# Optimization experiments

Hardware: AMD Instinct MI355X
Metric: run time of the kernel (lower is better)

## Reference

```python
import jax, jax.numpy as jnp
import numpy as np

BN_EPS = 1e-3  # keras BatchNormalization default epsilon

@jax.custom_vjp
def ste_sign(x):
    # larq ste_sign: sign(x) with sign(0) -> +1
    return jnp.where(x >= 0, 1.0, -1.0).astype(x.dtype)

def _ste_fwd(x):
    return ste_sign(x), x

def _ste_bwd(x, g):
    # straight-through estimator, gradient clipped to |x| <= 1
    return (g * (jnp.abs(x) <= 1).astype(g.dtype),)

ste_sign.defvjp(_ste_fwd, _ste_bwd)

def setup_inputs() -> dict:
    key = jax.random.key(0)
    k1, k2, k3, k4, k5, k6 = jax.random.split(key, 6)
    B, D_IN, D_H = 32768, 2048, 512
    return {
        "input_tensor": jax.random.normal(k1, (B, D_IN), dtype=jnp.float32),
        "W": jax.random.normal(k2, (D_IN, D_H), dtype=jnp.float32) * 0.05,
        "b": jax.random.normal(k3, (D_H,), dtype=jnp.float32) * 0.01,
        "beta": jax.random.normal(k4, (D_H,), dtype=jnp.float32) * 0.01,
        "moving_mean": jax.random.normal(k5, (D_H,), dtype=jnp.float32) * 0.1,
        "moving_var": jax.random.uniform(k6, (D_H,), dtype=jnp.float32, minval=0.5, maxval=1.5),
    }

def reference(input_tensor, W, b, beta, moving_mean, moving_var):
    # QuantDense: binarize input and kernel, float GEMM over {-1,+1} values
    xq = ste_sign(input_tensor)                # [B, D_in]
    wq = ste_sign(W)                           # [D_in, D_h]
    y = jnp.matmul(xq, wq) + b                 # [B, D_h]
    # BatchNorm inference (training=False), scale=False (no gamma), center=True
    inv = jax.lax.rsqrt(moving_var + BN_EPS)
    return (y - moving_mean) * inv + beta
```

## Files before the change

### kernel.cpp

```cpp
#include <hip/hip_runtime.h>
#include <stdint.h>

#define D_IN 2048
#define D_H  512
#define BM   64
#define NST  16

typedef __attribute__((ext_vector_type(4)))  int i32x4;
typedef __attribute__((ext_vector_type(16))) int i32x16;

__global__ __launch_bounds__(1024) void pack_wt_kernel(
    const float* __restrict__ W, char* __restrict__ Wf) {
  const int s = blockIdx.x;
  const int t = threadIdx.x >> 6;
  const int l = threadIdx.x & 63;
  const int n = t * 32 + (l & 31);
  const int kbase = s * 32 + 16 * (l >> 5);
  uint wq[4];
#pragma unroll
  for (int q = 0; q < 4; ++q) {
    uint w = 0x01010101u;
#pragma unroll
    for (int j = 0; j < 4; ++j) {
      uint bits = __float_as_uint(W[(size_t)(kbase + 4 * q + j) * D_H + n]);
      w ^= ((uint)((int)bits >> 31)) & (0xFEu << (8 * j));
    }
    wq[q] = w;
  }
  *(uint4*)(Wf + ((size_t)(s * 16 + t) * 64 + l) * 16) =
      make_uint4(wq[0], wq[1], wq[2], wq[3]);
}

__device__ __forceinline__ uint pack4(float4 v) {
  uint w = 0x01010101u;
  w ^= ((uint)((int)__float_as_uint(v.x) >> 31)) & 0x000000FEu;
  w ^= ((uint)((int)__float_as_uint(v.y) >> 31)) & 0x0000FE00u;
  w ^= ((uint)((int)__float_as_uint(v.z) >> 31)) & 0x00FE0000u;
  w ^= ((uint)((int)__float_as_uint(v.w) >> 31)) & 0xFE000000u;
  return w;
}

__global__ __launch_bounds__(512) void bgemm_kernel(
    const float* __restrict__ X, const char* __restrict__ Wf,
    const float* __restrict__ b, const float* __restrict__ beta,
    const float* __restrict__ mm, const float* __restrict__ mv,
    float* __restrict__ out) {
  __shared__ __align__(16) char XpL[2][8192];

  const int tid = threadIdx.x;
  const int l   = tid & 63;
  const int wv  = tid >> 6;
  const int am  = l & 31;
  const int ah  = l >> 5;
  const size_t m0 = (size_t)blockIdx.x * BM;
  const int colbase = wv * 64;

  const int r0 = tid >> 5;
  const int kw = tid & 31;
  const float* Xt = X + (m0 + r0) * D_IN + kw * 4;

  const int ws0 = r0 * 128 + (((kw >> 2) ^ (r0 & 7)) << 4) + (kw & 3) * 4;

  const int arow0 = am * 128;
  const int arow1 = arow0 + 32 * 128;
  const int akey  = am & 7;

  const char* Bb0 = Wf + (size_t)(2 * wv) * 1024 + (size_t)l * 16;
  const char* Bb1 = Bb0 + 1024;

  i32x16 acc00, acc01, acc10, acc11;
#pragma unroll
  for (int r = 0; r < 16; ++r) { acc00[r] = 0; acc01[r] = 0; acc10[r] = 0; acc11[r] = 0; }

  float4 P0a, P0b, P0c, P0d;
  float4 P1a, P1b, P1c, P1d;

  P0a = *(const float4*)(Xt);
  P0b = *(const float4*)(Xt + 16 * D_IN);
  P0c = *(const float4*)(Xt + 32 * D_IN);
  P0d = *(const float4*)(Xt + 48 * D_IN);
  P1a = *(const float4*)(Xt + 128);
  P1b = *(const float4*)(Xt + 128 + 16 * D_IN);
  P1c = *(const float4*)(Xt + 128 + 32 * D_IN);
  P1d = *(const float4*)(Xt + 128 + 48 * D_IN);
  *(uint*)(XpL[0] + ws0)        = pack4(P0a);
  *(uint*)(XpL[0] + ws0 + 2048) = pack4(P0b);
  *(uint*)(XpL[0] + ws0 + 4096) = pack4(P0c);
  *(uint*)(XpL[0] + ws0 + 6144) = pack4(P0d);
  __syncthreads();

#define STAGE_BODY(ST, Pca, Pcb, Pcc, Pcd, Pna, Pnb, Pnc, Pnd, PREF, PACKN)  \
  do {                                                                       \
    const char* buf = &XpL[(ST) & 1][0];                                     \
    const size_t so = (size_t)(ST) * 65536;                                  \
    i32x4 B0a = *(const i32x4*)(Bb0 + so + 0 * 16384);                       \
    i32x4 B0b = *(const i32x4*)(Bb1 + so + 0 * 16384);                       \
    i32x4 B1a = *(const i32x4*)(Bb0 + so + 1 * 16384);                       \
    i32x4 B1b = *(const i32x4*)(Bb1 + so + 1 * 16384);                       \
    i32x4 B2a = *(const i32x4*)(Bb0 + so + 2 * 16384);                       \
    i32x4 B2b = *(const i32x4*)(Bb1 + so + 2 * 16384);                       \
    i32x4 B3a = *(const i32x4*)(Bb0 + so + 3 * 16384);                       \
    i32x4 B3b = *(const i32x4*)(Bb1 + so + 3 * 16384);                       \
    if (PREF) {                                                              \
      const float* xp = Xt + ((ST) + 2) * 128;                               \
      Pna = *(const float4*)(xp);                                            \
      Pnb = *(const float4*)(xp + 16 * D_IN);                                \
      Pnc = *(const float4*)(xp + 32 * D_IN);                                \
      Pnd = *(const float4*)(xp + 48 * D_IN);                                \
    }                                                                        \
    if (PACKN) {     \
      char* nbuf = &XpL[((ST) + 1) & 1][0];                                  \
      *(uint*)(nbuf + ws0)        = pack4(Pca);                              \
      *(uint*)(nbuf + ws0 + 2048) = pack4(Pcb);                              \
      *(uint*)(nbuf + ws0 + 4096) = pack4(Pcc);                              \
      *(uint*)(nbuf + ws0 + 6144) = pack4(Pcd);                              \
    }                                                                        \
    {                                                                        \
      i32x4 a0 = *(const i32x4*)(buf + arow0 + (((0 + ah) ^ akey) << 4));    \
      i32x4 a1 = *(const i32x4*)(buf + arow1 + (((0 + ah) ^ akey) << 4));    \
      acc00 = __builtin_amdgcn_mfma_i32_32x32x32_i8(a0, B0a, acc00, 0, 0, 0);\
      acc10 = __builtin_amdgcn_mfma_i32_32x32x32_i8(a1, B0a, acc10, 0, 0, 0);\
      acc01 = __builtin_amdgcn_mfma_i32_32x32x32_i8(a0, B0b, acc01, 0, 0, 0);\
      acc11 = __builtin_amdgcn_mfma_i32_32x32x32_i8(a1, B0b, acc11, 0, 0, 0);\
    }                                                                        \
    {                                                                        \
      i32x4 a0 = *(const i32x4*)(buf + arow0 + (((2 + ah) ^ akey) << 4));    \
      i32x4 a1 = *(const i32x4*)(buf + arow1 + (((2 + ah) ^ akey) << 4));    \
      acc00 = __builtin_amdgcn_mfma_i32_32x32x32_i8(a0, B1a, acc00, 0, 0, 0);\
      acc10 = __builtin_amdgcn_mfma_i32_32x32x32_i8(a1, B1a, acc10, 0, 0, 0);\
      acc01 = __builtin_amdgcn_mfma_i32_32x32x32_i8(a0, B1b, acc01, 0, 0, 0);\
      acc11 = __builtin_amdgcn_mfma_i32_32x32x32_i8(a1, B1b, acc11, 0, 0, 0);\
    }                                                                        \
    {                                                                        \
      i32x4 a0 = *(const i32x4*)(buf + arow0 + (((4 + ah) ^ akey) << 4));    \
      i32x4 a1 = *(const i32x4*)(buf + arow1 + (((4 + ah) ^ akey) << 4));    \
      acc00 = __builtin_amdgcn_mfma_i32_32x32x32_i8(a0, B2a, acc00, 0, 0, 0);\
      acc10 = __builtin_amdgcn_mfma_i32_32x32x32_i8(a1, B2a, acc10, 0, 0, 0);\
      acc01 = __builtin_amdgcn_mfma_i32_32x32x32_i8(a0, B2b, acc01, 0, 0, 0);\
      acc11 = __builtin_amdgcn_mfma_i32_32x32x32_i8(a1, B2b, acc11, 0, 0, 0);\
    }                                                                        \
    {                                                                        \
      i32x4 a0 = *(const i32x4*)(buf + arow0 + (((6 + ah) ^ akey) << 4));    \
      i32x4 a1 = *(const i32x4*)(buf + arow1 + (((6 + ah) ^ akey) << 4));    \
      acc00 = __builtin_amdgcn_mfma_i32_32x32x32_i8(a0, B3a, acc00, 0, 0, 0);\
      acc10 = __builtin_amdgcn_mfma_i32_32x32x32_i8(a1, B3a, acc10, 0, 0, 0);\
      acc01 = __builtin_amdgcn_mfma_i32_32x32x32_i8(a0, B3b, acc01, 0, 0, 0);\
      acc11 = __builtin_amdgcn_mfma_i32_32x32x32_i8(a1, B3b, acc11, 0, 0, 0);\
    }                                                                        \
    __syncthreads();                                                         \
  } while (0)

#pragma unroll 1
  for (int st = 0; st < NST - 2; st += 2) {
    STAGE_BODY(st,     P1a, P1b, P1c, P1d, P0a, P0b, P0c, P0d, true, true);
    STAGE_BODY(st + 1, P0a, P0b, P0c, P0d, P1a, P1b, P1c, P1d, true, true);
  }
  STAGE_BODY(NST - 2, P1a, P1b, P1c, P1d, P0a, P0b, P0c, P0d, false, true);
  STAGE_BODY(NST - 1, P0a, P0b, P0c, P0d, P1a, P1b, P1c, P1d, false, false);
#undef STAGE_BODY

  const int rb = 4 * ah;
#pragma unroll
  for (int h = 0; h < 2; ++h) {
#pragma unroll
    for (int nt = 0; nt < 2; ++nt) {
      const i32x16 A = (h == 0) ? ((nt == 0) ? acc00 : acc01)
                                : ((nt == 0) ? acc10 : acc11);
      const int c = colbase + nt * 32 + am;
      const float bb  = b[c];
      const float mmc = mm[c];
      const float bec = beta[c];
      const float inv = rsqrtf(mv[c] + 1e-3f);
#pragma unroll
      for (int r = 0; r < 16; ++r) {
        const int row = (r & 3) + 8 * (r >> 2) + rb + 32 * h;
        out[(m0 + row) * D_H + c] = ((float)A[r] + bb - mmc) * inv + bec;
      }
    }
  }
}

extern "C" void kernel_launch(void* const* d_in, const int* in_sizes, int n_in,
                              void* d_out, int out_size, void* d_ws, size_t ws_size,
                              hipStream_t stream) {
  const float* X    = (const float*)d_in[0];
  const float* W    = (const float*)d_in[1];
  const float* b    = (const float*)d_in[2];
  const float* beta = (const float*)d_in[3];
  const float* mm   = (const float*)d_in[4];
  const float* mv   = (const float*)d_in[5];
  float* out = (float*)d_out;

  char* Wf = (char*)d_ws;

  pack_wt_kernel<<<dim3(D_IN / 32), dim3(1024), 0, stream>>>(W, Wf);

  const int M = in_sizes[0] / D_IN;
  bgemm_kernel<<<dim3(M / BM), dim3(512), 0, stream>>>(X, Wf, b, beta, mm, mv, out);
}
```

Before: 108.9 us.

## Halve K-stage depth and store packed X in MFMA-native LDS layout

Doubles the number of K stages so each stage covers 64 K-elements instead of 128, halving LDS buffers and per-thread prefetch registers. Each thread now loads contiguous float4s along a row, and packed bytes are written straight into the MFMA operand layout, so A fragments are read with a plain lane-indexed 16-byte load and no XOR swizzle. The aim is lower register and LDS pressure and simpler address math. The cost is twice as many __syncthreads barriers, less compute per barrier for hiding global-load latency, and possible bank conflicts on the unswizzled writes.

```diff
diff --git a/kernel.cpp b/kernel.cpp
--- a/kernel.cpp
+++ b/kernel.cpp
@@ -4,7 +4,7 @@
 #define D_IN 2048
 #define D_H  512
 #define BM   64
-#define NST  16
+#define NST  32
 
 typedef __attribute__((ext_vector_type(4)))  int i32x4;
 typedef __attribute__((ext_vector_type(16))) int i32x16;
@@ -45,7 +45,7 @@
     const float* __restrict__ b, const float* __restrict__ beta,
     const float* __restrict__ mm, const float* __restrict__ mv,
     float* __restrict__ out) {
-  __shared__ __align__(16) char XpL[2][8192];
+  __shared__ __align__(16) char XpL[2][4096];
 
   const int tid = threadIdx.x;
   const int l   = tid & 63;
@@ -55,15 +55,14 @@
   const size_t m0 = (size_t)blockIdx.x * BM;
   const int colbase = wv * 64;
 
-  const int r0 = tid >> 5;
-  const int kw = tid & 31;
-  const float* Xt = X + (m0 + r0) * D_IN + kw * 4;
+  const int xrow = tid >> 3;
+  const int c0   = tid & 7;
+  const float4* X4row = (const float4*)(X + (m0 + xrow) * D_IN);
 
-  const int ws0 = r0 * 128 + (((kw >> 2) ^ (r0 & 7)) << 4) + (kw & 3) * 4;
+  const int ws0 = (xrow >> 5) * 2048 + (((xrow & 31) + 32 * ((c0 >> 2) & 1)) << 4)
+                  + 4 * (c0 & 3);
 
-  const int arow0 = am * 128;
-  const int arow1 = arow0 + 32 * 128;
-  const int akey  = am & 7;
+  const int alane = l * 16;
 
   const char* Bb0 = Wf + (size_t)(2 * wv) * 1024 + (size_t)l * 16;
   const char* Bb1 = Bb0 + 1024;
@@ -72,91 +71,59 @@
 #pragma unroll
   for (int r = 0; r < 16; ++r) { acc00[r] = 0; acc01[r] = 0; acc10[r] = 0; acc11[r] = 0; }
 
-  float4 P0a, P0b, P0c, P0d;
-  float4 P1a, P1b, P1c, P1d;
+  float4 P0a, P0b, P1a, P1b;
 
-  P0a = *(const float4*)(Xt);
-  P0b = *(const float4*)(Xt + 16 * D_IN);
-  P0c = *(const float4*)(Xt + 32 * D_IN);
-  P0d = *(const float4*)(Xt + 48 * D_IN);
-  P1a = *(const float4*)(Xt + 128);
-  P1b = *(const float4*)(Xt + 128 + 16 * D_IN);
-  P1c = *(const float4*)(Xt + 128 + 32 * D_IN);
-  P1d = *(const float4*)(Xt + 128 + 48 * D_IN);
+  P0a = X4row[c0];
+  P0b = X4row[c0 + 8];
+  P1a = X4row[16 + c0];
+  P1b = X4row[16 + c0 + 8];
   *(uint*)(XpL[0] + ws0)        = pack4(P0a);
-  *(uint*)(XpL[0] + ws0 + 2048) = pack4(P0b);
-  *(uint*)(XpL[0] + ws0 + 4096) = pack4(P0c);
-  *(uint*)(XpL[0] + ws0 + 6144) = pack4(P0d);
+  *(uint*)(XpL[0] + ws0 + 1024) = pack4(P0b);
   __syncthreads();
 
-#define STAGE_BODY(ST, Pca, Pcb, Pcc, Pcd, Pna, Pnb, Pnc, Pnd, PREF, PACKN)  \
+#define STAGE_BODY(ST, Pca, Pcb, Pna, Pnb, PREF, PACKN)                      \
   do {                                                                       \
-    const char* buf = &XpL[(ST) & 1][0];                                     \
-    const size_t so = (size_t)(ST) * 65536;                                  \
-    i32x4 B0a = *(const i32x4*)(Bb0 + so + 0 * 16384);                       \
-    i32x4 B0b = *(const i32x4*)(Bb1 + so + 0 * 16384);                       \
-    i32x4 B1a = *(const i32x4*)(Bb0 + so + 1 * 16384);                       \
-    i32x4 B1b = *(const i32x4*)(Bb1 + so + 1 * 16384);                       \
-    i32x4 B2a = *(const i32x4*)(Bb0 + so + 2 * 16384);                       \
-    i32x4 B2b = *(const i32x4*)(Bb1 + so + 2 * 16384);                       \
-    i32x4 B3a = *(const i32x4*)(Bb0 + so + 3 * 16384);                       \
-    i32x4 B3b = *(const i32x4*)(Bb1 + so + 3 * 16384);                       \
+    const size_t so = (size_t)(ST) * 32768;                                  \
+    i32x4 B00 = *(const i32x4*)(Bb0 + so);                   \
+    i32x4 B01 = *(const i32x4*)(Bb1 + so);                   \
+    i32x4 B10 = *(const i32x4*)(Bb0 + so + 16384);           \
+    i32x4 B11 = *(const i32x4*)(Bb1 + so + 16384);           \
     if (PREF) {                                                              \
-      const float* xp = Xt + ((ST) + 2) * 128;                               \
-      Pna = *(const float4*)(xp);                                            \
-      Pnb = *(const float4*)(xp + 16 * D_IN);                                \
-      Pnc = *(const float4*)(xp + 32 * D_IN);                                \
-      Pnd = *(const float4*)(xp + 48 * D_IN);                                \
+      Pna = X4row[((ST) + 2) * 16 + c0];                                     \
+      Pnb = X4row[((ST) + 2) * 16 + c0 + 8];                                 \
     }                                                                        \
     if (PACKN) {     \
       char* nbuf = &XpL[((ST) + 1) & 1][0];                                  \
       *(uint*)(nbuf + ws0)        = pack4(Pca);                              \
-      *(uint*)(nbuf + ws0 + 2048) = pack4(Pcb);                              \
-      *(uint*)(nbuf + ws0 + 4096) = pack4(Pcc);                              \
-      *(uint*)(nbuf + ws0 + 6144) = pack4(Pcd);                              \
+      *(uint*)(nbuf + ws0 + 1024) = pack4(Pcb);                              \
+    }                                                                        \
+    const char* buf = &XpL[(ST) & 1][0];                                     \
+    {                                                                        \
+      i32x4 a0 = *(const i32x4*)(buf + alane);                   \
+      i32x4 a1 = *(const i32x4*)(buf + 2048 + alane);            \
+      acc00 = __builtin_amdgcn_mfma_i32_32x32x32_i8(a0, B00, acc00, 0, 0, 0);\
+      acc10 = __builtin_amdgcn_mfma_i32_32x32x32_i8(a1, B00, acc10, 0, 0, 0);\
+      acc01 = __builtin_amdgcn_mfma_i32_32x32x32_i8(a0, B01, acc01, 0, 0, 0);\
+      acc11 = __builtin_amdgcn_mfma_i32_32x32x32_i8(a1, B01, acc11, 0, 0, 0);\
     }                                                                        \
     {                                                                        \
-      i32x4 a0 = *(const i32x4*)(buf + arow0 + (((0 + ah) ^ akey) << 4));    \
-      i32x4 a1 = *(const i32x4*)(buf + arow1 + (((0 + ah) ^ akey) << 4));    \
-      acc00 = __builtin_amdgcn_mfma_i32_32x32x32_i8(a0, B0a, acc00, 0, 0, 0);\
-      acc10 = __builtin_amdgcn_mfma_i32_32x32x32_i8(a1, B0a, acc10, 0, 0, 0);\
-      acc01 = __builtin_amdgcn_mfma_i32_32x32x32_i8(a0, B0b, acc01, 0, 0, 0);\
-      acc11 = __builtin_amdgcn_mfma_i32_32x32x32_i8(a1, B0b, acc11, 0, 0, 0);\
-    }                                                                        \
-    {                                                                        \
-      i32x4 a0 = *(const i32x4*)(buf + arow0 + (((2 + ah) ^ akey) << 4));    \
-      i32x4 a1 = *(const i32x4*)(buf + arow1 + (((2 + ah) ^ akey) << 4));    \
-      acc00 = __builtin_amdgcn_mfma_i32_32x32x32_i8(a0, B1a, acc00, 0, 0, 0);\
-      acc10 = __builtin_amdgcn_mfma_i32_32x32x32_i8(a1, B1a, acc10, 0, 0, 0);\
-      acc01 = __builtin_amdgcn_mfma_i32_32x32x32_i8(a0, B1b, acc01, 0, 0, 0);\
-      acc11 = __builtin_amdgcn_mfma_i32_32x32x32_i8(a1, B1b, acc11, 0, 0, 0);\
-    }                                                                        \
-    {                                                                        \
-      i32x4 a0 = *(const i32x4*)(buf + arow0 + (((4 + ah) ^ akey) << 4));    \
-      i32x4 a1 = *(const i32x4*)(buf + arow1 + (((4 + ah) ^ akey) << 4));    \
-      acc00 = __builtin_amdgcn_mfma_i32_32x32x32_i8(a0, B2a, acc00, 0, 0, 0);\
-      acc10 = __builtin_amdgcn_mfma_i32_32x32x32_i8(a1, B2a, acc10, 0, 0, 0);\
-      acc01 = __builtin_amdgcn_mfma_i32_32x32x32_i8(a0, B2b, acc01, 0, 0, 0);\
-      acc11 = __builtin_amdgcn_mfma_i32_32x32x32_i8(a1, B2b, acc11, 0, 0, 0);\
-    }                                                                        \
-    {                                                                        \
-      i32x4 a0 = *(const i32x4*)(buf + arow0 + (((6 + ah) ^ akey) << 4));    \
-      i32x4 a1 = *(const i32x4*)(buf + arow1 + (((6 + ah) ^ akey) << 4));    \
-      acc00 = __builtin_amdgcn_mfma_i32_32x32x32_i8(a0, B3a, acc00, 0, 0, 0);\
-      acc10 = __builtin_amdgcn_mfma_i32_32x32x32_i8(a1, B3a, acc10, 0, 0, 0);\
-      acc01 = __builtin_amdgcn_mfma_i32_32x32x32_i8(a0, B3b, acc01, 0, 0, 0);\
-      acc11 = __builtin_amdgcn_mfma_i32_32x32x32_i8(a1, B3b, acc11, 0, 0, 0);\
+      i32x4 a0 = *(const i32x4*)(buf + 1024 + alane);            \
+      i32x4 a1 = *(const i32x4*)(buf + 2048 + 1024 + alane);     \
+      acc00 = __builtin_amdgcn_mfma_i32_32x32x32_i8(a0, B10, acc00, 0, 0, 0);\
+      acc10 = __builtin_amdgcn_mfma_i32_32x32x32_i8(a1, B10, acc10, 0, 0, 0);\
+      acc01 = __builtin_amdgcn_mfma_i32_32x32x32_i8(a0, B11, acc01, 0, 0, 0);\
+      acc11 = __builtin_amdgcn_mfma_i32_32x32x32_i8(a1, B11, acc11, 0, 0, 0);\
     }                                                                        \
     __syncthreads();                                                         \
   } while (0)
 
 #pragma unroll 1
   for (int st = 0; st < NST - 2; st += 2) {
-    STAGE_BODY(st,     P1a, P1b, P1c, P1d, P0a, P0b, P0c, P0d, true, true);
-    STAGE_BODY(st + 1, P0a, P0b, P0c, P0d, P1a, P1b, P1c, P1d, true, true);
+    STAGE_BODY(st,     P1a, P1b, P0a, P0b, true, true);
+    STAGE_BODY(st + 1, P0a, P0b, P1a, P1b, true, true);
   }
-  STAGE_BODY(NST - 2, P1a, P1b, P1c, P1d, P0a, P0b, P0c, P0d, false, true);
-  STAGE_BODY(NST - 1, P0a, P0b, P0c, P0d, P1a, P1b, P1c, P1d, false, false);
+  STAGE_BODY(NST - 2, P1a, P1b, P0a, P0b, false, true);
+  STAGE_BODY(NST - 1, P0a, P0b, P1a, P1b, false, false);
 #undef STAGE_BODY
 
   const int rb = 4 * ah;
```

New measurement: 93.92 us. 13.8% less time.
